# Optimization experiments

Measured on AMD Instinct MI355X. Metric: run time of the kernel, lower is better.

Reference implementation:

```python
import jax, jax.numpy as jnp
import numpy as np

S, B, T = 500, 128, 250          # encoder steps, batch, decoder text_len
H, K, V, VOCAB = 512, 128, 128, 1000
NEG = -1e9


def _lstm_cell(x, h, c, w_ih, w_hh, b_ih, b_hh):
    # torch.nn.LSTMCell gate order: i, f, g, o
    gates = x @ w_ih.T + b_ih + h @ w_hh.T + b_hh
    i, f, g, o = jnp.split(gates, 4, axis=-1)
    c_new = jax.nn.sigmoid(f) * c + jax.nn.sigmoid(i) * jnp.tanh(g)
    h_new = jax.nn.sigmoid(o) * jnp.tanh(c_new)
    return h_new, c_new


def setup_inputs():
    root = jax.random.key(0)
    ks = jax.random.split(root, 12)
    w = lambda k, shape, fan: (jax.random.normal(k, shape, jnp.float32) / np.sqrt(fan))
    inp = {
        'key': jax.random.normal(ks[0], (S, B, K), jnp.float32),
        'values': jax.random.normal(ks[1], (S, B, V), jnp.float32),
        'lens': jnp.maximum(jax.random.randint(ks[2], (B,), 0, S), 1),
        'text': jax.random.randint(ks[3], (T, B), 0, VOCAB),
        # embedding, padding_idx=0 -> row 0 zeroed
        'emb': w(ks[4], (VOCAB, H), H).at[0].set(0.0),
        # lstm1: input hidden_dim + value_size -> hidden H
        'w_ih1': w(ks[5], (4 * H, H + V), H + V),
        'w_hh1': w(ks[6], (4 * H, H), H),
        'b_ih1': jnp.zeros((4 * H,), jnp.float32),
        'b_hh1': jnp.zeros((4 * H,), jnp.float32),
        # lstm2: input H -> key_size K
        'w_ih2': w(ks[7], (4 * K, H), H),
        'w_hh2': w(ks[8], (4 * K, K), K),
        'b_ih2': jnp.zeros((4 * K,), jnp.float32),
        'b_hh2': jnp.zeros((4 * K,), jnp.float32),
        # character_prob: (key_size+value_size) -> vocab
        'w_out': w(ks[9], (VOCAB, K + V), K + V),
        'b_out': jnp.zeros((VOCAB,), jnp.float32),
    }
    return inp


def reference(key, values, lens, text, emb, w_ih1, w_hh1, b_ih1, b_hh1,
              w_ih2, w_hh2, b_ih2, b_hh2, w_out, b_out):
    key_t = jnp.transpose(key, (1, 0, 2))      # [B,S,K]
    val_t = jnp.transpose(values, (1, 0, 2))   # [B,S,V]
    mask = jnp.arange(S)[None, :] >= lens[:, None]  # [B,S] True = padded

    # teacher forcing ratio == 1: step 0 uses embedding(argmax(zeros)) = row 0,
    # steps i>=1 use embeddings[i]. Precompute the whole input sequence.
    embs = emb[text]  # [T,B,H]
    step0 = jnp.broadcast_to(emb[0], (1, B, H))
    char_seq = jnp.concatenate([step0, embs[1:T - 1]], axis=0)  # [T-1,B,H]

    def step(carry, char_embed):
        h1, c1, h2, c2, context = carry
        inp = jnp.concatenate([char_embed, context], axis=1)        # [B,H+V]
        h1, c1 = _lstm_cell(inp, h1, c1, w_ih1, w_hh1, b_ih1, b_hh1)
        h2, c2 = _lstm_cell(h1, h2, c2, w_ih2, w_hh2, b_ih2, b_hh2)  # query [B,K]
        energy = jnp.einsum('bsk,bk->bs', key_t, h2)
        energy = jnp.where(mask, NEG, energy)
        attn = jax.nn.softmax(energy, axis=1)
        context = jnp.einsum('bs,bsv->bv', attn, val_t)              # [B,V]
        pred = jnp.concatenate([h2, context], axis=1) @ w_out.T + b_out
        return (h1, c1, h2, c2, context), pred

    z = lambda d: jnp.zeros((B, d), jnp.float32)
    init = (z(H), z(H), z(K), z(K), z(V))
    _, preds = jax.lax.scan(step, init, char_seq)   # [T-1,B,VOCAB]
    return jnp.transpose(preds, (1, 0, 2))          # [B,T-1,VOCAB]
```

## Files before the change

### kernel.cpp

```cpp
#include <hip/hip_runtime.h>
#include <hip/hip_bf16.h>

typedef unsigned short u16;
typedef unsigned long long u64;
typedef short short8 __attribute__((ext_vector_type(8)));
typedef float f32x4 __attribute__((ext_vector_type(4)));

#define S_ 500
#define B_ 128
#define T_ 250
#define H_ 512
#define K_ 128
#define V_ 128
#define VOC 1000
#define NSTEP 249
#define NWG 160
#define NROW 128

#define VSH_BYTES   128000
#define H1ST_STRIDE 520
#define ALIAS_BYTES 33280
#define SMEM_BYTES  (VSH_BYTES + ALIAS_BYTES)

#define FA    0
#define FB    128
#define FC    192
#define FINIT 384

__device__ __forceinline__ float bf2f(u16 u) {
    union { unsigned int i; float f; } x; x.i = ((unsigned int)u) << 16; return x.f;
}
__device__ __forceinline__ u16 f2bf(float f) {
    union { float f; unsigned int i; } x; x.f = f;
    unsigned int r = x.i + 0x7fffu + ((x.i >> 16) & 1u);
    return (u16)(r >> 16);
}
__device__ __forceinline__ float sigm(float x) { return 1.f / (1.f + __expf(-x)); }
__device__ __forceinline__ float tanh_f(float x) { return 2.f / (1.f + __expf(-2.f * x)) - 1.f; }
__device__ __forceinline__ f32x4 mfma16(short8 a, short8 b, f32x4 c) {
    return __builtin_amdgcn_mfma_f32_16x16x32_bf16(a, b, c, 0, 0, 0);
}

__device__ __forceinline__ u64 ld_state8(const u16* p) {
    return __hip_atomic_load((const u64*)p, __ATOMIC_RELAXED, __HIP_MEMORY_SCOPE_AGENT);
}
__device__ __forceinline__ short8 ld_state16(const u16* p) {
    union { u64 q[2]; short8 s; } u;
    u.q[0] = ld_state8(p); u.q[1] = ld_state8(p + 4);
    return u.s;
}
__device__ __forceinline__ unsigned ld_state4(const u16* p) {
    return __hip_atomic_load((const unsigned*)p, __ATOMIC_RELAXED, __HIP_MEMORY_SCOPE_AGENT);
}
__device__ __forceinline__ void st_state4(u16* p, unsigned v) {
    __hip_atomic_store((unsigned*)p, v, __ATOMIC_RELAXED, __HIP_MEMORY_SCOPE_AGENT);
}
__device__ __forceinline__ void st_pair(u16* p, float a, float b) {
    st_state4(p, (unsigned)f2bf(a) | ((unsigned)f2bf(b) << 16));
}

__device__ __forceinline__ void set_flag(unsigned* f, unsigned tag) {
    __syncthreads();
    if (threadIdx.x == 0)
        __hip_atomic_store(f, tag, __ATOMIC_RELAXED, __HIP_MEMORY_SCOPE_AGENT);
}
__device__ __forceinline__ void wait_flags(const unsigned* f, int n, unsigned tag) {
    if ((int)threadIdx.x < n) {
        while (__hip_atomic_load(f + threadIdx.x, __ATOMIC_RELAXED,
                                 __HIP_MEMORY_SCOPE_AGENT) < tag)
            __builtin_amdgcn_s_sleep(1);
    }
    __syncthreads();
}

__global__ __launch_bounds__(256) void pack_kernel(
    const float* __restrict__ w_ih1, const float* __restrict__ w_hh1,
    const float* __restrict__ b_ih1, const float* __restrict__ b_hh1,
    const float* __restrict__ w_ih2, const float* __restrict__ w_hh2,
    const float* __restrict__ b_ih2, const float* __restrict__ b_hh2,
    const float* __restrict__ w_out, const float* __restrict__ emb,
    u16* __restrict__ W1f, u16* __restrict__ W2f, u16* __restrict__ Woutf,
    float* __restrict__ bias1, float* __restrict__ bias2, u16* __restrict__ emb_bf,
    unsigned* __restrict__ bar)
{
    const int i0 = blockIdx.x * 256 + threadIdx.x;
    const int stride = gridDim.x * 256;
    for (int i = i0; i < 1024; i += stride)
        __hip_atomic_store(bar + i, 0u, __ATOMIC_RELAXED, __HIP_MEMORY_SCOPE_AGENT);
    for (int i = i0; i < 1152 * 2048; i += stride) {
        int k = i >> 11, n = i & 2047;
        float v = (k < 640) ? w_ih1[n * 640 + k] : w_hh1[n * 512 + (k - 640)];
        W1f[((size_t)(k >> 3) * 2048 + n) * 8 + (k & 7)] = f2bf(v);
    }
    for (int i = i0; i < 640 * 512; i += stride) {
        int k = i >> 9, n = i & 511;
        float v = (k < 512) ? w_ih2[n * 512 + k] : w_hh2[n * 128 + (k - 512)];
        W2f[((size_t)(k >> 3) * 512 + n) * 8 + (k & 7)] = f2bf(v);
    }
    for (int i = i0; i < 256 * 1024; i += stride) {
        int k = i >> 10, n = i & 1023;
        float v = (n < VOC) ? w_out[n * 256 + k] : 0.f;
        Woutf[((size_t)(k >> 3) * 1024 + n) * 8 + (k & 7)] = f2bf(v);
    }
    for (int i = i0; i < 2048; i += stride) bias1[i] = b_ih1[i] + b_hh1[i];
    for (int i = i0; i < 512; i += stride) bias2[i] = b_ih2[i] + b_hh2[i];
    for (int i = i0; i < VOC * H_; i += stride) emb_bf[i] = f2bf(emb[i]);
}

__global__ __launch_bounds__(256) void conv_kv_kernel(
    const float* __restrict__ key, const float* __restrict__ values,
    u16* __restrict__ key_bf, u16* __restrict__ val_bf)
{
    const int i0 = blockIdx.x * 256 + threadIdx.x;
    const int stride = gridDim.x * 256;
    for (int i = i0; i < S_ * B_ * K_; i += stride) {
        int s = i >> 14;
        int r = i & 16383;
        int b = r >> 7, k = r & 127;
        size_t d = ((size_t)b * S_ + s) * K_ + k;
        key_bf[d] = f2bf(key[i]);
        val_bf[d] = f2bf(values[i]);
    }
}

__global__ __launch_bounds__(256, 1) void decoder_kernel(
    const u16* __restrict__ emb_bf, const int* __restrict__ text,
    const u16* __restrict__ W1f, const float* __restrict__ bias1,
    const u16* __restrict__ W2f, const float* __restrict__ bias2,
    const u16* __restrict__ key_bf, const u16* __restrict__ val_bf,
    const int* __restrict__ lens,
    u16* __restrict__ CT, u16* __restrict__ H1, u16* __restrict__ H2,
    u16* __restrict__ Hc, unsigned* __restrict__ bar)
{
    extern __shared__ char smem[];
    u16*   vshare = (u16*)smem;
    char*  alias  = smem + VSH_BYTES;
    u16*   h1st   = (u16*)alias;
    float* Gb     = (float*)alias;
    float* ebuf   = (float*)alias;
    float* cbuf   = (float*)(alias + 2048);
    float* h2s    = (float*)(alias + 4096);
    float* redm   = (float*)(alias + 4608);

    const int wg = blockIdx.x;
    const int tid = threadIdx.x;
    const int lane = tid & 63, wv = tid >> 6;
    const int lrow = lane & 15, lk = lane >> 4;
    const bool isrow = wg < NROW;

    const int mh1 = wg >> 5, hg1 = wg & 31;
    const int n1 = wv * 512 + hg1 * 16 + lrow;
    const int l2 = wg - NROW;
    const int q2 = l2 >> 3, hg2 = l2 & 7;
    const int n2 = wv * 128 + hg2 * 16 + lrow;
    const int b  = wg;
    const int mylen = isrow ? lens[b] : 0;

    float c1r[2] = {0.f, 0.f};
    float c2r[2] = {0.f, 0.f};
    f32x4 acc1[2] = {{0,0,0,0},{0,0,0,0}};
    f32x4 acc2[2] = {{0,0,0,0},{0,0,0,0}};

    {
        int i0 = wg * 256 + tid, stride = NWG * 256;
        for (int i = i0; i < B_ * V_ / 2; i += stride) st_state4(CT + 2 * i, 0u);
        for (int i = i0; i < B_ * H_ / 2; i += stride) st_state4(H1 + 2 * i, 0u);
        for (int i = i0; i < B_ * K_;     i += stride) st_state4(H2 + 2 * i, 0u);
        if (isrow) {
            const u16* vp = val_bf + (size_t)b * S_ * V_;
            for (int i = tid; i < (S_ * V_) / 8; i += 256)
                *reinterpret_cast<short8*>(vshare + i * 8) =
                    *reinterpret_cast<const short8*>(vp + (size_t)i * 8);
        }
    }
    set_flag(bar + FINIT + wg, 1u);
    wait_flags(bar + FINIT, NWG, 1u);

    for (int t = 0; t < NSTEP; ++t) {
        const int nxt = (t & 1) ^ 1;
        u16* H2n = H2 + (size_t)nxt * B_ * K_;
        const unsigned tg = (unsigned)(t + 1);

        if (isrow) {
            wait_flags(bar + FC + mh1 * 32, 32, (unsigned)t);
            int grow[2];
#pragma unroll
            for (int rt = 0; rt < 2; ++rt) grow[rt] = mh1 * 32 + rt * 16 + lrow;
#pragma unroll
            for (int kc = 16; kc < 20; ++kc) {
                int k = kc * 32 + lk * 8;
                short8 bw = *reinterpret_cast<const short8*>(W1f + ((size_t)(k >> 3) * 2048 + n1) * 8);
#pragma unroll
                for (int rt = 0; rt < 2; ++rt) {
                    short8 a = ld_state16(CT + grow[rt] * V_ + (k - 512));
                    acc1[rt] = mfma16(a, bw, acc1[rt]);
                }
            }
            float bv = bias1[n1];
#pragma unroll
            for (int rt = 0; rt < 2; ++rt)
#pragma unroll
                for (int j = 0; j < 4; ++j)
                    Gb[(rt * 16 + lk * 4 + j) * 65 + wv * 16 + lrow] = acc1[rt][j] + bv;
            __syncthreads();
            {
                int rb = tid >> 3, j0 = (tid & 7) * 2;
                int bb = mh1 * 32 + rb;
                float gi0 = Gb[rb * 65 + j0],      gf0 = Gb[rb * 65 + 16 + j0];
                float gg0 = Gb[rb * 65 + 32 + j0], go0 = Gb[rb * 65 + 48 + j0];
                float gi1 = Gb[rb * 65 + j0 + 1],      gf1 = Gb[rb * 65 + 16 + j0 + 1];
                float gg1 = Gb[rb * 65 + 32 + j0 + 1], go1 = Gb[rb * 65 + 48 + j0 + 1];
                float cn0 = sigm(gf0) * c1r[0] + sigm(gi0) * tanh_f(gg0);
                float cn1 = sigm(gf1) * c1r[1] + sigm(gi1) * tanh_f(gg1);
                c1r[0] = cn0; c1r[1] = cn1;
                st_pair(H1 + bb * H_ + hg1 * 16 + j0,
                        sigm(go0) * tanh_f(cn0), sigm(go1) * tanh_f(cn1));
            }
            set_flag(bar + FA + wg, tg);

            acc1[0] = (f32x4){0,0,0,0}; acc1[1] = (f32x4){0,0,0,0};
            const u16* aemb[2];
#pragma unroll
            for (int rt = 0; rt < 2; ++rt) {
                int tok = text[(t + 1) * B_ + grow[rt]];
                aemb[rt] = emb_bf + (size_t)tok * H_;
            }
#pragma unroll 4
            for (int kc = 0; kc < 16; ++kc) {
                int k = kc * 32 + lk * 8;
                short8 bw = *reinterpret_cast<const short8*>(W1f + ((size_t)(k >> 3) * 2048 + n1) * 8);
#pragma unroll
                for (int rt = 0; rt < 2; ++rt) {
                    short8 a = *reinterpret_cast<const short8*>(aemb[rt] + k);
                    acc1[rt] = mfma16(a, bw, acc1[rt]);
                }
            }
            wait_flags(bar + FA + mh1 * 32, 32, tg);
            {
                const u16* src = H1 + (size_t)(mh1 * 32) * H_;
#pragma unroll
                for (int it = 0; it < 8; ++it) {
                    int c = it * 256 + tid;
                    int row = c >> 6, col = (c & 63) * 8;
                    u64 lo = ld_state8(src + (size_t)row * H_ + col);
                    u64 hi = ld_state8(src + (size_t)row * H_ + col + 4);
                    u64* dst = (u64*)(h1st + row * H1ST_STRIDE + col);
                    dst[0] = lo; dst[1] = hi;
                }
            }
            __syncthreads();
#pragma unroll 4
            for (int kc = 20; kc < 36; ++kc) {
                int k = kc * 32 + lk * 8;
                short8 bw = *reinterpret_cast<const short8*>(W1f + ((size_t)(k >> 3) * 2048 + n1) * 8);
#pragma unroll
                for (int rt = 0; rt < 2; ++rt) {
                    short8 a = *reinterpret_cast<const short8*>(
                        h1st + (rt * 16 + lrow) * H1ST_STRIDE + (kc - 20) * 32 + lk * 8);
                    acc1[rt] = mfma16(a, bw, acc1[rt]);
                }
            }

            wait_flags(bar + FB + mh1 * 8, 8, tg);
            u16* Hc_t = Hc + (size_t)t * B_ * 256;
            if (tid < 64) {
                unsigned v = ld_state4(H2n + b * K_ + 2 * tid);
                h2s[2 * tid]     = bf2f((u16)(v & 0xffffu));
                h2s[2 * tid + 1] = bf2f((u16)(v >> 16));
                *reinterpret_cast<unsigned*>(Hc_t + b * 256 + 2 * tid) = v;
            }
            __syncthreads();

            for (int s = tid; s < 512; s += 256) {
                float e = -1e9f;
                if (s < S_) {
                    const u16* kp = key_bf + ((size_t)b * S_ + s) * K_;
                    float a = 0.f;
#pragma unroll
                    for (int kk = 0; kk < K_; kk += 8) {
                        short8 kv = *reinterpret_cast<const short8*>(kp + kk);
#pragma unroll
                        for (int j = 0; j < 8; ++j)
                            a += bf2f((u16)kv[j]) * h2s[kk + j];
                    }
                    e = (s < mylen) ? a : -1e9f;
                }
                ebuf[s] = e;
            }
            __syncthreads();

            float m = fmaxf(ebuf[tid], ebuf[tid + 256]);
#pragma unroll
            for (int off = 32; off > 0; off >>= 1) m = fmaxf(m, __shfl_down(m, off));
            if (lane == 0) redm[wv] = m;
            __syncthreads();
            const float maxv = fmaxf(fmaxf(redm[0], redm[1]), fmaxf(redm[2], redm[3]));

            float psum = 0.f;
            for (int s = tid; s < 512; s += 256) {
                float pv = __expf(ebuf[s] - maxv);
                ebuf[s] = pv;
                psum += pv;
            }
#pragma unroll
            for (int off = 32; off > 0; off >>= 1) psum += __shfl_down(psum, off);
            if (lane == 0) redm[4 + wv] = psum;
            __syncthreads();
            const float rinv = 1.f / (redm[4] + redm[5] + redm[6] + redm[7]);

            const int s0 = wv * 125;
            float p0 = 0.f, p1 = 0.f;
            for (int s = s0; s < s0 + 125; ++s) {
                float w = ebuf[s];
                unsigned pk = *reinterpret_cast<const unsigned*>(vshare + s * V_ + lane * 2);
                p0 += w * bf2f((u16)(pk & 0xffffu));
                p1 += w * bf2f((u16)(pk >> 16));
            }
            cbuf[wv * V_ + lane * 2]     = p0;
            cbuf[wv * V_ + lane * 2 + 1] = p1;
            __syncthreads();

            if (tid < 64) {
                int v0 = 2 * tid, v1 = 2 * tid + 1;
                float ctx0 = (cbuf[v0] + cbuf[V_ + v0] + cbuf[2 * V_ + v0] + cbuf[3 * V_ + v0]) * rinv;
                float ctx1 = (cbuf[v1] + cbuf[V_ + v1] + cbuf[2 * V_ + v1] + cbuf[3 * V_ + v1]) * rinv;
                st_pair(CT + b * V_ + v0, ctx0, ctx1);
                *reinterpret_cast<unsigned*>(Hc_t + b * 256 + K_ + v0) =
                    (unsigned)f2bf(ctx0) | ((unsigned)f2bf(ctx1) << 16);
            }
            set_flag(bar + FC + wg, tg);
        } else {
            wait_flags(bar + FA + q2 * 32, 32, tg);
            {
                const u16* src = H1 + (size_t)(q2 * 32) * H_;
#pragma unroll
                for (int it = 0; it < 8; ++it) {
                    int c = it * 256 + tid;
                    int row = c >> 6, col = (c & 63) * 8;
                    u64 lo = ld_state8(src + (size_t)row * H_ + col);
                    u64 hi = ld_state8(src + (size_t)row * H_ + col + 4);
                    u64* dst = (u64*)(h1st + row * H1ST_STRIDE + col);
                    dst[0] = lo; dst[1] = hi;
                }
            }
            __syncthreads();
#pragma unroll 4
            for (int kc = 0; kc < 16; ++kc) {
                int k = kc * 32 + lk * 8;
                short8 bw = *reinterpret_cast<const short8*>(W2f + ((size_t)(k >> 3) * 512 + n2) * 8);
#pragma unroll
                for (int rt = 0; rt < 2; ++rt) {
                    short8 a = *reinterpret_cast<const short8*>(
                        h1st + (rt * 16 + lrow) * H1ST_STRIDE + kc * 32 + lk * 8);
                    acc2[rt] = mfma16(a, bw, acc2[rt]);
                }
            }
            float bv = bias2[n2];
            __syncthreads();
#pragma unroll
            for (int rt = 0; rt < 2; ++rt)
#pragma unroll
                for (int j = 0; j < 4; ++j)
                    Gb[(rt * 16 + lk * 4 + j) * 65 + wv * 16 + lrow] = acc2[rt][j] + bv;
            __syncthreads();
            {
                int rb = tid >> 3, j0 = (tid & 7) * 2;
                int bb = q2 * 32 + rb;
                float gi0 = Gb[rb * 65 + j0],      gf0 = Gb[rb * 65 + 16 + j0];
                float gg0 = Gb[rb * 65 + 32 + j0], go0 = Gb[rb * 65 + 48 + j0];
                float gi1 = Gb[rb * 65 + j0 + 1],      gf1 = Gb[rb * 65 + 16 + j0 + 1];
                float gg1 = Gb[rb * 65 + 32 + j0 + 1], go1 = Gb[rb * 65 + 48 + j0 + 1];
                float cn0 = sigm(gf0) * c2r[0] + sigm(gi0) * tanh_f(gg0);
                float cn1 = sigm(gf1) * c2r[1] + sigm(gi1) * tanh_f(gg1);
                c2r[0] = cn0; c2r[1] = cn1;
                st_pair(H2n + bb * K_ + hg2 * 16 + j0,
                        sigm(go0) * tanh_f(cn0), sigm(go1) * tanh_f(cn1));
            }
            set_flag(bar + FB + l2, tg);

            wait_flags(bar + FB + q2 * 8, 8, tg);
            acc2[0] = (f32x4){0,0,0,0}; acc2[1] = (f32x4){0,0,0,0};
#pragma unroll
            for (int kc = 16; kc < 20; ++kc) {
                int k = kc * 32 + lk * 8;
                short8 bw = *reinterpret_cast<const short8*>(W2f + ((size_t)(k >> 3) * 512 + n2) * 8);
#pragma unroll
                for (int rt = 0; rt < 2; ++rt) {
                    short8 a = ld_state16(H2n + (q2 * 32 + rt * 16 + lrow) * K_ + (k - 512));
                    acc2[rt] = mfma16(a, bw, acc2[rt]);
                }
            }
        }
    }
}

__global__ __launch_bounds__(256) void k4_kernel(
    const u16* __restrict__ Hc, const u16* __restrict__ Woutf,
    const float* __restrict__ b_out, float* __restrict__ out)
{
    const int bx = blockIdx.x;
    const int mt = bx >> 4, nt = bx & 15;
    const int tid = threadIdx.x;
    const int lane = tid & 63, g = tid >> 6;
    const int lrow = lane & 15, lk = lane >> 4;
    const int n = nt * 64 + g * 16 + lrow;
    const float bias = (n < VOC) ? b_out[n] : 0.f;

    f32x4 acc[8];
#pragma unroll
    for (int rt = 0; rt < 8; ++rt) acc[rt] = (f32x4){bias, bias, bias, bias};

#pragma unroll
    for (int kc = 0; kc < 8; ++kc) {
        int k = kc * 32 + lk * 8;
        short8 bw = *reinterpret_cast<const short8*>(Woutf + ((size_t)(k >> 3) * 1024 + n) * 8);
#pragma unroll
        for (int rt = 0; rt < 8; ++rt) {
            int R = mt * 128 + rt * 16 + lrow;
            short8 a = *reinterpret_cast<const short8*>(Hc + (size_t)R * 256 + k);
            acc[rt] = mfma16(a, bw, acc[rt]);
        }
    }
    if (n < VOC) {
#pragma unroll
        for (int rt = 0; rt < 8; ++rt)
#pragma unroll
            for (int j = 0; j < 4; ++j) {
                int R = mt * 128 + rt * 16 + lk * 4 + j;
                int tt = R >> 7, bb = R & 127;
                out[((size_t)bb * NSTEP + tt) * VOC + n] = acc[rt][j];
            }
    }
}

extern "C" void kernel_launch(void* const* d_in, const int* in_sizes, int n_in,
                              void* d_out, int out_size, void* d_ws, size_t ws_size,
                              hipStream_t stream)
{
    const float* key    = (const float*)d_in[0];
    const float* values = (const float*)d_in[1];
    const int*   lens   = (const int*)d_in[2];
    const int*   text   = (const int*)d_in[3];
    const float* emb    = (const float*)d_in[4];
    const float* w_ih1  = (const float*)d_in[5];
    const float* w_hh1  = (const float*)d_in[6];
    const float* b_ih1  = (const float*)d_in[7];
    const float* b_hh1  = (const float*)d_in[8];
    const float* w_ih2  = (const float*)d_in[9];
    const float* w_hh2  = (const float*)d_in[10];
    const float* b_ih2  = (const float*)d_in[11];
    const float* b_hh2  = (const float*)d_in[12];
    const float* w_out  = (const float*)d_in[13];
    const float* b_out  = (const float*)d_in[14];

    char* p = (char*)d_ws;
    auto alloc = [&](size_t bytes) -> char* {
        char* r = p;
        p += (bytes + 255) & ~(size_t)255;
        return r;
    };
    u16*      key_bf = (u16*)     alloc((size_t)B_ * S_ * K_ * 2);
    u16*      val_bf = (u16*)     alloc((size_t)B_ * S_ * V_ * 2);
    u16*      emb_bf = (u16*)     alloc((size_t)VOC * H_ * 2);
    u16*      W1f    = (u16*)     alloc((size_t)1152 * 2048 * 2);
    u16*      W2f    = (u16*)     alloc((size_t)640 * 512 * 2);
    u16*      Woutf  = (u16*)     alloc((size_t)256 * 1024 * 2);
    float*    bias1  = (float*)   alloc(2048 * 4);
    float*    bias2  = (float*)   alloc(512 * 4);
    u16*      CT     = (u16*)     alloc((size_t)B_ * V_ * 2);
    u16*      H1     = (u16*)     alloc((size_t)B_ * H_ * 2);
    u16*      H2     = (u16*)     alloc((size_t)2 * B_ * K_ * 2);
    u16*      Hc     = (u16*)     alloc((size_t)NSTEP * B_ * 256 * 2);
    unsigned* bar    = (unsigned*)alloc(4096);
    (void)ws_size; (void)in_sizes; (void)n_in; (void)out_size;

    hipFuncSetAttribute((const void*)decoder_kernel,
                        hipFuncAttributeMaxDynamicSharedMemorySize, SMEM_BYTES);

    pack_kernel<<<512, 256, 0, stream>>>(w_ih1, w_hh1, b_ih1, b_hh1,
                                         w_ih2, w_hh2, b_ih2, b_hh2,
                                         w_out, emb, W1f, W2f, Woutf, bias1, bias2, emb_bf,
                                         bar);
    conv_kv_kernel<<<4096, 256, 0, stream>>>(key, values, key_bf, val_bf);

    decoder_kernel<<<NWG, 256, SMEM_BYTES, stream>>>(emb_bf, text, W1f, bias1, W2f, bias2,
                                                     key_bf, val_bf, lens, CT, H1, H2, Hc, bar);

    k4_kernel<<<NSTEP * 16, 256, 0, stream>>>(Hc, Woutf, b_out, (float*)d_out);
}
```

Baseline: 5.377 ms.

## Prefetch weights and keys before flag waits, fuse energy into registers

Moves the W1 context-weight loads and the first quarter of each key row ahead of the cross-workgroup flag waits, so those global loads overlap the spin time. The energy computation now keeps both scores in registers, reads h2 as float4 vectors, and drops the ebuf round-trip along with one __syncthreads. The context accumulation loop is split into two independent accumulator chains to expose more ILP. This raises register pressure (prefetched short8 arrays), which could hurt occupancy on the persistent kernel.

```diff
diff --git a/kernel.cpp b/kernel.cpp
--- a/kernel.cpp
+++ b/kernel.cpp
@@ -182,18 +182,22 @@
         const unsigned tg = (unsigned)(t + 1);
 
         if (isrow) {
+            int grow[2];
+#pragma unroll
+            for (int rt = 0; rt < 2; ++rt) grow[rt] = mh1 * 32 + rt * 16 + lrow;
+            short8 bwc[4];
+#pragma unroll
+            for (int kc = 16; kc < 20; ++kc)
+                bwc[kc - 16] = *reinterpret_cast<const short8*>(
+                    W1f + ((size_t)(kc * 4 + lk) * 2048 + n1) * 8);
             wait_flags(bar + FC + mh1 * 32, 32, (unsigned)t);
-            int grow[2];
-#pragma unroll
-            for (int rt = 0; rt < 2; ++rt) grow[rt] = mh1 * 32 + rt * 16 + lrow;
 #pragma unroll
             for (int kc = 16; kc < 20; ++kc) {
                 int k = kc * 32 + lk * 8;
-                short8 bw = *reinterpret_cast<const short8*>(W1f + ((size_t)(k >> 3) * 2048 + n1) * 8);
 #pragma unroll
                 for (int rt = 0; rt < 2; ++rt) {
                     short8 a = ld_state16(CT + grow[rt] * V_ + (k - 512));
-                    acc1[rt] = mfma16(a, bw, acc1[rt]);
+                    acc1[rt] = mfma16(a, bwc[kc - 16], acc1[rt]);
                 }
             }
             float bv = bias1[n1];
@@ -261,6 +265,15 @@
                 }
             }
 
+            const int s1 = tid + 256;
+            const u16* kp0 = key_bf + ((size_t)b * S_ + tid) * K_;
+            const u16* kp1 = key_bf + ((size_t)b * S_ + (s1 < S_ ? s1 : 0)) * K_;
+            short8 kpre0[4], kpre1[4];
+#pragma unroll
+            for (int c = 0; c < 4; ++c) {
+                kpre0[c] = *reinterpret_cast<const short8*>(kp0 + c * 8);
+                kpre1[c] = *reinterpret_cast<const short8*>(kp1 + c * 8);
+            }
             wait_flags(bar + FB + mh1 * 8, 8, tg);
             u16* Hc_t = Hc + (size_t)t * B_ * 256;
             if (tid < 64) {
@@ -271,37 +284,42 @@
             }
             __syncthreads();
 
-            for (int s = tid; s < 512; s += 256) {
-                float e = -1e9f;
-                if (s < S_) {
-                    const u16* kp = key_bf + ((size_t)b * S_ + s) * K_;
-                    float a = 0.f;
-#pragma unroll
-                    for (int kk = 0; kk < K_; kk += 8) {
-                        short8 kv = *reinterpret_cast<const short8*>(kp + kk);
-#pragma unroll
-                        for (int j = 0; j < 8; ++j)
-                            a += bf2f((u16)kv[j]) * h2s[kk + j];
+            float e0 = 0.f, e1 = 0.f;
+#pragma unroll
+            for (int kb = 0; kb < 4; ++kb) {
+                f32x4 hv[8];
+#pragma unroll
+                for (int j = 0; j < 8; ++j)
+                    hv[j] = *reinterpret_cast<const f32x4*>(&h2s[kb * 32 + j * 4]);
+#pragma unroll
+                for (int c = 0; c < 4; ++c) {
+                    short8 k0 = (kb == 0) ? kpre0[c]
+                              : *reinterpret_cast<const short8*>(kp0 + kb * 32 + c * 8);
+                    short8 k1 = (kb == 0) ? kpre1[c]
+                              : *reinterpret_cast<const short8*>(kp1 + kb * 32 + c * 8);
+#pragma unroll
+                    for (int j = 0; j < 8; ++j) {
+                        float h = hv[c * 2 + (j >> 2)][j & 3];
+                        e0 += bf2f((u16)k0[j]) * h;
+                        e1 += bf2f((u16)k1[j]) * h;
                     }
-                    e = (s < mylen) ? a : -1e9f;
-                }
-                ebuf[s] = e;
-            }
-            __syncthreads();
-
-            float m = fmaxf(ebuf[tid], ebuf[tid + 256]);
+                }
+            }
+            e0 = (tid < mylen) ? e0 : -1e9f;
+            e1 = (s1 < mylen) ? e1 : -1e9f;
+
+            float m = fmaxf(e0, e1);
 #pragma unroll
             for (int off = 32; off > 0; off >>= 1) m = fmaxf(m, __shfl_down(m, off));
             if (lane == 0) redm[wv] = m;
             __syncthreads();
             const float maxv = fmaxf(fmaxf(redm[0], redm[1]), fmaxf(redm[2], redm[3]));
 
-            float psum = 0.f;
-            for (int s = tid; s < 512; s += 256) {
-                float pv = __expf(ebuf[s] - maxv);
-                ebuf[s] = pv;
-                psum += pv;
-            }
+            float p0v = __expf(e0 - maxv);
+            float p1v = __expf(e1 - maxv);
+            ebuf[tid] = p0v;
+            ebuf[s1]  = p1v;
+            float psum = p0v + p1v;
 #pragma unroll
             for (int off = 32; off > 0; off >>= 1) psum += __shfl_down(psum, off);
             if (lane == 0) redm[4 + wv] = psum;
@@ -309,15 +327,25 @@
             const float rinv = 1.f / (redm[4] + redm[5] + redm[6] + redm[7]);
 
             const int s0 = wv * 125;
-            float p0 = 0.f, p1 = 0.f;
-            for (int s = s0; s < s0 + 125; ++s) {
-                float w = ebuf[s];
-                unsigned pk = *reinterpret_cast<const unsigned*>(vshare + s * V_ + lane * 2);
-                p0 += w * bf2f((u16)(pk & 0xffffu));
-                p1 += w * bf2f((u16)(pk >> 16));
-            }
-            cbuf[wv * V_ + lane * 2]     = p0;
-            cbuf[wv * V_ + lane * 2 + 1] = p1;
+            float pa0 = 0.f, pa1 = 0.f, pb0 = 0.f, pb1 = 0.f;
+            for (int s = s0; s < s0 + 124; s += 2) {
+                float w0 = ebuf[s];
+                unsigned pk0 = *reinterpret_cast<const unsigned*>(vshare + s * V_ + lane * 2);
+                pa0 += w0 * bf2f((u16)(pk0 & 0xffffu));
+                pa1 += w0 * bf2f((u16)(pk0 >> 16));
+                float w1 = ebuf[s + 1];
+                unsigned pk1 = *reinterpret_cast<const unsigned*>(vshare + (s + 1) * V_ + lane * 2);
+                pb0 += w1 * bf2f((u16)(pk1 & 0xffffu));
+                pb1 += w1 * bf2f((u16)(pk1 >> 16));
+            }
+            {
+                float w = ebuf[s0 + 124];
+                unsigned pk = *reinterpret_cast<const unsigned*>(vshare + (s0 + 124) * V_ + lane * 2);
+                pa0 += w * bf2f((u16)(pk & 0xffffu));
+                pa1 += w * bf2f((u16)(pk >> 16));
+            }
+            cbuf[wv * V_ + lane * 2]     = pa0 + pb0;
+            cbuf[wv * V_ + lane * 2 + 1] = pa1 + pb1;
             __syncthreads();
 
             if (tid < 64) {
```

Result: slower. 5.486 ms (+2.0%).
